# Optimization experiments

Measured on AMD Instinct MI355X. Metric: run time of the kernel, lower is better.

Reference implementation:

```python
import jax, jax.numpy as jnp
import numpy as np

N, E, D, H, L = 50000, 400000, 128, 256, 2
ZR = 0.8          # z_ratio
GN_EPS = 1e-5     # PyG GraphNorm eps


def _graph_norm(x, w, b, a):
    # PyG GraphNorm on a single graph: x - mean_scale*mean, rms-normalize
    mu = jnp.mean(x, axis=0, keepdims=True)
    xc = x - a * mu
    var = jnp.mean(xc * xc, axis=0, keepdims=True)
    return w * xc / jnp.sqrt(var + GN_EPS) + b


def _gat(x, src, dst, W, a_src, a_dst, bias):
    # PyG GATConv, heads=1, add_self_loops=True, negative_slope=0.2.
    # edge_dim is None -> edge_attr is ignored by the layer.
    n = x.shape[0]
    loop = jnp.arange(n)
    s = jnp.concatenate([src, loop])   # [E+N]
    d = jnp.concatenate([dst, loop])
    xw = x @ W.T                        # [N,H]
    logit = jax.nn.leaky_relu((xw @ a_src)[s] + (xw @ a_dst)[d], 0.2)
    m = jax.ops.segment_max(logit, d, num_segments=n)
    ex = jnp.exp(logit - m[d])
    den = jax.ops.segment_sum(ex, d, num_segments=n)
    alpha = ex / (den[d] + 1e-16)
    return jax.ops.segment_sum(alpha[:, None] * xw[s], d, num_segments=n) + bias


def _mix(x0, x1, mask):
    return jnp.where(mask, ZR * x1 + (1.0 - ZR) * x0, ZR * x0 + (1.0 - ZR) * x1)


def _forward(x_, edge_index, edge_attr, question_embeddings, subgraph_mask,
             node_in_W, node_in_b, edge_in_W, edge_in_b, q_in_W, q_in_b,
             nqm_W, nqm_b, eqm_W, eqm_b,
             t0_W, t0_b, t1_W, t1_b,
             gat_W, gat_asrc, gat_adst, gat_bias,
             cgn_w, cgn_b, cgn_a,
             c0_W, c0_b, c1_W, c1_b,
             gn_w, gn_b, gn_a, final_W, final_b):
    src, dst = edge_index[0], edge_index[1]
    mask = subgraph_mask[:, None]
    x = jax.nn.relu(x_ @ node_in_W.T + node_in_b)                 # [N,H]
    e = jax.nn.relu(edge_attr @ edge_in_W.T + edge_in_b)          # [E,H] (unused by GAT: lin_edge is None)
    q = jax.nn.relu(question_embeddings @ q_in_W.T + q_in_b)[0]   # [1,H]
    n = x.shape[0]
    for l in range(L):
        qx = jnp.broadcast_to(q, (n, H))
        xc = jax.nn.relu(jnp.concatenate([x, qx], axis=-1) @ nqm_W[l].T + nqm_b[l])
        # torch also computes e_combined = relu(edge_question_mix([e,q])) but GATConv
        # (edge_dim=None) ignores it, so it is dead code: omitted.
        x1 = jax.nn.relu(xc @ t1_W[l].T + t1_b[l])
        x0 = jax.nn.relu(xc @ t0_W[l].T + t0_b[l])
        h = _mix(x0, x1, mask)
        h = _gat(h, src, dst, gat_W[l], gat_asrc[l], gat_adst[l], gat_bias[l])
        h = _graph_norm(h, cgn_w[l], cgn_b[l], cgn_a[l])
        # dropout p=0 -> no-op
        hc = jnp.concatenate([h, xc], axis=-1)                    # [N,2H]
        x1 = hc @ c1_W[l].T + c1_b[l]
        x0 = hc @ c0_W[l].T + c0_b[l]
        x = _mix(x0, x1, mask)
        x = _graph_norm(x, gn_w[l], gn_b[l], gn_a[l])
    # masked mean/max/add pooling over subgraph nodes (single graph)
    mk = mask.astype(x.dtype)
    cnt = jnp.sum(mk)
    x_add = jnp.sum(x * mk, axis=0, keepdims=True)
    x_mean = x_add / jnp.maximum(cnt, 1.0)
    x_max = jnp.max(jnp.where(mask, x, -jnp.inf), axis=0, keepdims=True)
    pooled = jnp.concatenate([x_mean, x_max, x_add], axis=-1)     # [1,3H]
    return pooled @ final_W.T + final_b                           # [1,H]


def setup_inputs() -> dict:
    keys = jax.random.split(jax.random.key(0), 64)
    it = iter(range(64))
    def nx(shape, s=0.05):
        return jax.random.normal(keys[next(it)], shape, jnp.float32) * s
    inp = {}
    inp['x_'] = jax.random.normal(keys[next(it)], (N, D), jnp.float32)
    inp['edge_index'] = jax.random.randint(keys[next(it)], (2, E), 0, N)
    inp['edge_attr'] = jax.random.normal(keys[next(it)], (E, D), jnp.float32)
    inp['question_embeddings'] = jax.random.normal(keys[next(it)], (1, 1, D), jnp.float32)
    inp['subgraph_mask'] = jax.random.bernoulli(keys[next(it)], 0.5, (N,))
    inp['node_in_W'] = nx((H, D)); inp['node_in_b'] = nx((H,))
    inp['edge_in_W'] = nx((H, D)); inp['edge_in_b'] = nx((H,))
    inp['q_in_W'] = nx((H, D));    inp['q_in_b'] = nx((H,))
    inp['nqm_W'] = nx((L, H, 2 * H)); inp['nqm_b'] = nx((L, H))
    inp['eqm_W'] = nx((L, H, 2 * H)); inp['eqm_b'] = nx((L, H))
    inp['t0_W'] = nx((L, H, H)); inp['t0_b'] = nx((L, H))
    inp['t1_W'] = nx((L, H, H)); inp['t1_b'] = nx((L, H))
    inp['gat_W'] = nx((L, H, H)); inp['gat_asrc'] = nx((L, H))
    inp['gat_adst'] = nx((L, H)); inp['gat_bias'] = nx((L, H))
    inp['cgn_w'] = jnp.ones((L, H)); inp['cgn_b'] = jnp.zeros((L, H)); inp['cgn_a'] = jnp.ones((L, H))
    inp['c0_W'] = nx((L, H, 2 * H)); inp['c0_b'] = nx((L, H))
    inp['c1_W'] = nx((L, H, 2 * H)); inp['c1_b'] = nx((L, H))
    inp['gn_w'] = jnp.ones((L, H)); inp['gn_b'] = jnp.zeros((L, H)); inp['gn_a'] = jnp.ones((L, H))
    inp['final_W'] = nx((H, 3 * H)); inp['final_b'] = nx((H,))
    return inp


def reference(x_, edge_index, edge_attr, question_embeddings, subgraph_mask,
              node_in_W, node_in_b, edge_in_W, edge_in_b, q_in_W, q_in_b,
              nqm_W, nqm_b, eqm_W, eqm_b,
              t0_W, t0_b, t1_W, t1_b,
              gat_W, gat_asrc, gat_adst, gat_bias,
              cgn_w, cgn_b, cgn_a,
              c0_W, c0_b, c1_W, c1_b,
              gn_w, gn_b, gn_a, final_W, final_b):
    return _forward(x_, edge_index, edge_attr, question_embeddings, subgraph_mask,
                    node_in_W, node_in_b, edge_in_W, edge_in_b, q_in_W, q_in_b,
                    nqm_W, nqm_b, eqm_W, eqm_b,
                    t0_W, t0_b, t1_W, t1_b,
                    gat_W, gat_asrc, gat_adst, gat_bias,
                    cgn_w, cgn_b, cgn_a,
                    c0_W, c0_b, c1_W, c1_b,
                    gn_w, gn_b, gn_a, final_W, final_b)
```

## Files before the change

kernel.cpp:

```cpp
#include <hip/hip_runtime.h>
#include <stdint.h>

#define NNODES 50000
#define NEDGES 400000
#define MPAD   50048
#define MTILES 391
#define ZRF    0.8f
#define GNEPS  1e-5f
#define NBLK   196

typedef unsigned short u16;
typedef __bf16 bf16x8 __attribute__((ext_vector_type(8)));
typedef float  f32x4  __attribute__((ext_vector_type(4)));

#define OFF_NODEW 0
#define OFF_NQM   32768
#define OFF_TCAT  163840
#define OFF_GAT   425984
#define OFF_CCAT  557056
#define W_TOTAL   1081344

__device__ __forceinline__ float b2f(u16 u){ union{uint32_t i; float f;} x; x.i=((uint32_t)u)<<16; return x.f; }
__device__ __forceinline__ u16 f2b(float f){ union{float f; uint32_t i;} x; x.f=f; uint32_t r=x.i+0x7FFFu+((x.i>>16)&1u); return (u16)(r>>16); }
__device__ __forceinline__ float lrelu(float x){ return x>0.f? x : 0.2f*x; }
__device__ __forceinline__ void atomicMaxF(float* a, float v){
  if (v>=0.f) atomicMax((int*)a, __float_as_int(v));
  else atomicMin((unsigned int*)a, (unsigned int)__float_as_int(v));
}

__device__ __forceinline__ void gl16(const void* g, void* l){
  __builtin_amdgcn_global_load_lds((const __attribute__((address_space(1))) void*)g,
                                   (__attribute__((address_space(3))) void*)l, 16, 0, 0);
}
__device__ __forceinline__ void bar(){
  __builtin_amdgcn_sched_barrier(0);
  asm volatile("" ::: "memory");
  __builtin_amdgcn_s_barrier();
  asm volatile("" ::: "memory");
  __builtin_amdgcn_sched_barrier(0);
}

template<int DUAL,int SPLIT,int RELU,int STATS,int DOTAV>
__device__ __forceinline__ void gemm_body(const u16* __restrict__ A0, const u16* __restrict__ A1,
    int ldA, const u16* __restrict__ B, const float* __restrict__ bias,
    u16* __restrict__ out, int ldo, int NT, int K,
    const uint32_t* __restrict__ mask, float* __restrict__ sums,
    const float* __restrict__ asrc, const float* __restrict__ adst,
    float* __restrict__ avs, float* __restrict__ avd)
{
  __shared__ alignas(16) char smem[DUAL ? 33792 : 34816];
  char* sm = smem;
  float* was = (float*)(smem + 32768);
  float* val = was + 128;

  const int tid  = threadIdx.x;
  const int nwg = gridDim.x;
  const int qc = nwg >> 3, rc = nwg & 7;
  const int xcd = blockIdx.x & 7, xi = blockIdx.x >> 3;
  const int lt = (xcd < rc ? xcd * (qc + 1) : rc * (qc + 1) + (xcd - rc) * qc) + xi;
  const int bm0 = (lt / NT) * 128;
  const int bn0 = (lt % NT) * (DUAL ? 64 : 128);

  if (DUAL && tid < 128) {
    int gr = bm0 + tid;
    int mk = (gr < NNODES) ? (mask[gr] != 0) : 0;
    was[tid] = mk ? ZRF : (1.0f - ZRF);
    val[tid] = (gr < NNODES) ? 1.0f : 0.0f;
  }

  const int lane = tid & 63;
  const int wv   = tid >> 6;
  const int wm   = (wv >> 1) * 64;
  const int wn   = (wv & 1) * (DUAL ? 32 : 64);
  const int lrow = lane & 15;
  const int kg16 = (lane >> 4) * 16;
  const int swz  = ((lrow >> 1) & 3) << 4;

  const int rA  = ((wv << 6) + lane) >> 2;
  const int gsw = (((lane & 3) ^ ((rA >> 1) & 3)) << 3);
  const u16* pa  = A0 + (size_t)(bm0 + rA) * ldA + gsw;
  const u16* pa2 = pa + 64 * ldA;
  const u16* pa1  = SPLIT ? (A1 + (size_t)(bm0 + rA) * 256 + gsw) : nullptr;
  const u16* pa12 = SPLIT ? (pa1 + 64 * 256) : nullptr;
  const u16* pb0 = B + (size_t)(bn0 + rA) * K + gsw;
  const u16* pb1 = DUAL ? (B + (size_t)(256 + bn0 + rA) * K + gsw) : (pb0 + (size_t)64 * K);
  const int dA0 = wv * 1024, dA1 = 4096 + wv * 1024;
  const int dB0 = 8192 + wv * 1024, dB1 = 12288 + wv * 1024;

  const int KT = K >> 5;
  f32x4 acc[DUAL ? 2 : 1][4][DUAL ? 2 : 4] = {};

#define STAGE(bb, ktv) do { \
    int ks_ = (ktv) * 32; \
    const u16 *qa_, *qa2_; \
    if (SPLIT && ks_ >= 256) { qa_ = pa1 + (ks_ - 256); qa2_ = pa12 + (ks_ - 256); } \
    else                     { qa_ = pa + ks_;           qa2_ = pa2 + ks_; } \
    char* db_ = sm + (bb); \
    gl16(qa_,       db_ + dA0); \
    gl16(qa2_,      db_ + dA1); \
    gl16(pb0 + ks_, db_ + dB0); \
    gl16(pb1 + ks_, db_ + dB1); \
  } while (0)

  STAGE(0, 0);
  int bb = 0;
  for (int kt = 0; kt < KT; ++kt) {
    if (kt + 1 < KT) { STAGE(bb ^ 16384, kt + 1); asm volatile("s_waitcnt vmcnt(4)" ::: "memory"); }
    else             { asm volatile("s_waitcnt vmcnt(0)" ::: "memory"); }
    bar();
    const char* Ab = sm + bb;
    const char* Bb = Ab + 8192;
    bf16x8 af[4];
#pragma unroll
    for (int mi = 0; mi < 4; ++mi)
      af[mi] = *(const bf16x8*)(Ab + (wm + mi * 16 + lrow) * 64 + (kg16 ^ swz));
    if (DUAL) {
#pragma unroll
      for (int ni = 0; ni < 2; ++ni) {
        int ro = (wn + ni * 16 + lrow) * 64 + (kg16 ^ swz);
        bf16x8 b0 = *(const bf16x8*)(Bb + ro);
        bf16x8 b1 = *(const bf16x8*)(Bb + 4096 + ro);
#pragma unroll
        for (int mi = 0; mi < 4; ++mi) {
          acc[0][mi][ni] = __builtin_amdgcn_mfma_f32_16x16x32_bf16(af[mi], b0, acc[0][mi][ni], 0, 0, 0);
          acc[DUAL?1:0][mi][ni] = __builtin_amdgcn_mfma_f32_16x16x32_bf16(af[mi], b1, acc[DUAL?1:0][mi][ni], 0, 0, 0);
        }
      }
    } else {
#pragma unroll
      for (int ni = 0; ni < (DUAL ? 2 : 4); ++ni) {
        bf16x8 bv = *(const bf16x8*)(Bb + (wn + ni * 16 + lrow) * 64 + (kg16 ^ swz));
#pragma unroll
        for (int mi = 0; mi < 4; ++mi)
          acc[0][mi][ni] = __builtin_amdgcn_mfma_f32_16x16x32_bf16(af[mi], bv, acc[0][mi][ni], 0, 0, 0);
      }
    }
    bar();
    bb ^= 16384;
  }
#undef STAGE

  const int rb = (lane >> 4) * 4;
  u16* ep = (u16*)smem;
  if (DUAL) {
    float sA[2] = {0, 0}, qA[2] = {0, 0};
#pragma unroll
    for (int ni = 0; ni < 2; ++ni) {
      int coll = wn + ni * 16 + lrow;
      float b1v = bias[bn0 + coll];
      float b0v = bias[256 + bn0 + coll];
#pragma unroll
      for (int mi = 0; mi < 4; ++mi) {
        int rowl = wm + mi * 16 + rb;
#pragma unroll
        for (int r = 0; r < 4; ++r) {
          float v1 = acc[0][mi][ni][r] + b1v;
          float v0 = acc[DUAL?1:0][mi][ni][r] + b0v;
          if (RELU) { v1 = fmaxf(v1, 0.f); v0 = fmaxf(v0, 0.f); }
          float wa = was[rowl + r];
          float v = wa * v1 + (1.0f - wa) * v0;
          if (STATS) { float vl = val[rowl + r]; sA[ni] += v * vl; qA[ni] += v * v * vl; }
          ep[(rowl + r) * 72 + coll] = f2b(v);
        }
      }
    }
    bar();
#pragma unroll
    for (int p = 0; p < 4; ++p) {
      int rowl = p * 32 + (tid >> 3);
      uint4 v = *(const uint4*)&ep[rowl * 72 + (tid & 7) * 8];
      *(uint4*)&out[(size_t)(bm0 + rowl) * ldo + bn0 + (tid & 7) * 8] = v;
    }
    if (STATS) {
#pragma unroll
      for (int ni = 0; ni < 2; ++ni) {
        sA[ni] += __shfl_xor(sA[ni], 16); sA[ni] += __shfl_xor(sA[ni], 32);
        qA[ni] += __shfl_xor(qA[ni], 16); qA[ni] += __shfl_xor(qA[ni], 32);
      }
      if (lane < 16) {
#pragma unroll
        for (int ni = 0; ni < 2; ++ni) {
          int gc = bn0 + wn + ni * 16 + lane;
          atomicAdd(&sums[gc], sA[ni]);
          atomicAdd(&sums[256 + gc], qA[ni]);
        }
      }
    }
  } else {
    float sp[4][4] = {}, dp[4][4] = {};
#pragma unroll
    for (int ni = 0; ni < 4; ++ni) {
      int coll = wn + ni * 16 + lrow;
      float bv = bias ? bias[bn0 + coll] : 0.f;
      float as_ = 0.f, ad_ = 0.f;
      if (DOTAV) { as_ = asrc[bn0 + coll]; ad_ = adst[bn0 + coll]; }
#pragma unroll
      for (int mi = 0; mi < 4; ++mi) {
        int rowl = wm + mi * 16 + rb;
#pragma unroll
        for (int r = 0; r < 4; ++r) {
          float v = acc[0][mi][ni][r] + bv;
          if (RELU) v = fmaxf(v, 0.f);
          if (DOTAV) { sp[mi][r] += v * as_; dp[mi][r] += v * ad_; }
          ep[(rowl + r) * 132 + coll] = f2b(v);
        }
      }
    }
    bar();
#pragma unroll
    for (int p = 0; p < 8; ++p) {
      int rowl = p * 16 + (tid >> 4);
      uint4 v = *(const uint4*)&ep[rowl * 132 + (tid & 15) * 8];
      *(uint4*)&out[(size_t)(bm0 + rowl) * ldo + bn0 + (tid & 15) * 8] = v;
    }
    if (DOTAV) {
#pragma unroll
      for (int mi = 0; mi < 4; ++mi)
#pragma unroll
        for (int r = 0; r < 4; ++r) {
          float s_ = sp[mi][r], d_ = dp[mi][r];
          s_ += __shfl_xor(s_, 1); s_ += __shfl_xor(s_, 2); s_ += __shfl_xor(s_, 4); s_ += __shfl_xor(s_, 8);
          d_ += __shfl_xor(d_, 1); d_ += __shfl_xor(d_, 2); d_ += __shfl_xor(d_, 4); d_ += __shfl_xor(d_, 8);
          if (lrow == 0) {
            int row = bm0 + wm + mi * 16 + (lane >> 4) * 4 + r;
            atomicAdd(&avs[row], s_);
            atomicAdd(&avd[row], d_);
          }
        }
    }
  }
}

__global__ __launch_bounds__(256, 3) void g_nin(const u16* __restrict__ A, const u16* __restrict__ W,
    const float* __restrict__ b, u16* __restrict__ o)
{ gemm_body<0,0,1,0,0>(A, nullptr, 128, W, b, o, 256, 2, 128, nullptr, nullptr, nullptr, nullptr, nullptr, nullptr); }

__global__ __launch_bounds__(256, 3) void g_nqm(const u16* __restrict__ A, const u16* __restrict__ W,
    const float* __restrict__ b, u16* __restrict__ o)
{ gemm_body<0,0,1,0,0>(A, nullptr, 256, W, b, o, 256, 2, 256, nullptr, nullptr, nullptr, nullptr, nullptr, nullptr); }

__global__ __launch_bounds__(256, 3) void g_gat(const u16* __restrict__ A, const u16* __restrict__ W,
    u16* __restrict__ o, const float* __restrict__ asrc, const float* __restrict__ adst,
    float* __restrict__ avs, float* __restrict__ avd)
{ gemm_body<0,0,0,0,1>(A, nullptr, 256, W, nullptr, o, 256, 2, 256, nullptr, nullptr, asrc, adst, avs, avd); }

__global__ __launch_bounds__(256, 3) void g_tcat(const u16* __restrict__ A, const u16* __restrict__ W,
    const float* __restrict__ b, u16* __restrict__ o, const uint32_t* __restrict__ mask)
{ gemm_body<1,0,1,0,0>(A, nullptr, 256, W, b, o, 256, 4, 256, mask, nullptr, nullptr, nullptr, nullptr, nullptr); }

__global__ __launch_bounds__(256, 3) void g_ccat(const u16* __restrict__ A0, const u16* __restrict__ A1,
    const u16* __restrict__ W, const float* __restrict__ b, u16* __restrict__ o,
    const uint32_t* __restrict__ mask, float* __restrict__ sums)
{ gemm_body<1,1,0,1,0>(A0, A1, 256, W, b, o, 256, 4, 512, mask, sums, nullptr, nullptr, nullptr, nullptr); }

__global__ void foldw(const u16* __restrict__ Ws, const float* __restrict__ bs,
                      const float* __restrict__ scale, const float* __restrict__ shift,
                      int K, u16* __restrict__ Wd, float* __restrict__ bd){
  int n = blockIdx.x, t = threadIdx.x;
  float bacc = 0.f;
  for (int k = t; k < K; k += 256) {
    float w = b2f(Ws[(size_t)n * K + k]);
    if (k < 256) { bacc += w * shift[k]; w *= scale[k]; }
    Wd[(size_t)n * K + k] = f2b(w);
  }
  for (int d = 32; d; d >>= 1) bacc += __shfl_xor(bacc, d);
  __shared__ float red[4];
  if ((t & 63) == 0) red[t >> 6] = bacc;
  __syncthreads();
  if (t == 0) bd[n] = bs[n] + red[0] + red[1] + red[2] + red[3];
}

__global__ void zeroall(float* __restrict__ z, int ztot, float* __restrict__ pmax){
  int i = blockIdx.x * 256 + threadIdx.x;
  if (i < 256) pmax[i] = -__builtin_inff();
  for (int j = i; j < ztot; j += gridDim.x * 256) z[j] = 0.f;
}

__global__ void convw(const float* __restrict__ nodeW, const float* __restrict__ nqmW,
                      const float* __restrict__ t0W, const float* __restrict__ t1W,
                      const float* __restrict__ gatW, const float* __restrict__ c0W,
                      const float* __restrict__ c1W, u16* __restrict__ arena){
  int idx = blockIdx.x*256 + threadIdx.x;
  if (idx >= W_TOTAL) return;
  float v;
  if (idx < OFF_NQM) { v = nodeW[idx]; }
  else if (idx < OFF_TCAT){ int i = idx - OFF_NQM;  int l=i>>16; int r=(i>>8)&255; int k=i&255; v = nqmW[l*131072 + r*512 + k]; }
  else if (idx < OFF_GAT) { int i = idx - OFF_TCAT; int l=i>>17; int n=(i>>8)&511; int k=i&255;
                            const float* s = (n<256)? t1W : t0W; v = s[l*65536 + (n&255)*256 + k]; }
  else if (idx < OFF_CCAT){ int i = idx - OFF_GAT;  v = gatW[i]; }
  else                    { int i = idx - OFF_CCAT; int l=i>>18; int n=(i>>9)&511; int k=i&511;
                            const float* s = (n<256)? c1W : c0W; v = s[l*131072 + (n&255)*512 + k]; }
  arena[idx] = f2b(v);
}

__global__ void convxin(const float* __restrict__ x, u16* __restrict__ o){
  int idx = blockIdx.x*256 + threadIdx.x;
  if (idx >= MPAD*32) return;
  int n = idx >> 5; int c = (idx & 31)*4;
  float4 v = make_float4(0.f,0.f,0.f,0.f);
  if (n < NNODES) v = *(const float4*)&x[(size_t)n*128 + c];
  ushort4 r; r.x=f2b(v.x); r.y=f2b(v.y); r.z=f2b(v.z); r.w=f2b(v.w);
  *(ushort4*)&o[(size_t)n*128 + c] = r;
}

__global__ void biascat(const float* __restrict__ t1b, const float* __restrict__ t0b,
                        const float* __restrict__ c1b, const float* __restrict__ c0b,
                        float* __restrict__ tb, float* __restrict__ cb){
  int i = blockIdx.x*256 + threadIdx.x;
  if (i >= 2048) return;
  int which = i >> 10; int j = i & 1023; int l = j >> 9; int n = j & 511;
  const float* b1 = which ? c1b : t1b;
  const float* b0 = which ? c0b : t0b;
  float v = (n < 256) ? b1[l*256 + n] : b0[l*256 + n - 256];
  (which ? cb : tb)[l*512 + n] = v;
}

__global__ void qvk(const float* __restrict__ qemb, const float* __restrict__ W,
                    const float* __restrict__ b, float* __restrict__ qv){
  int h = threadIdx.x;
  float acc = b[h];
  for (int d = 0; d < 128; ++d) acc += qemb[d] * W[h*128 + d];
  qv[h] = fmaxf(acc, 0.f);
}

__global__ void qbk(const float* __restrict__ nqmW, const float* __restrict__ nqmB,
                    const float* __restrict__ qv, float* __restrict__ qb){
  int l = blockIdx.x, h = threadIdx.x;
  const float* wr = nqmW + l*131072 + h*512 + 256;
  float acc = nqmB[l*256 + h];
  for (int j = 0; j < 256; ++j) acc += wr[j] * qv[j];
  qb[l*256 + h] = acc;
}

__global__ void detmask(const unsigned char* __restrict__ mb, int* __restrict__ flag){
  __shared__ int cnt_s;
  if (threadIdx.x == 0) cnt_s = 0;
  __syncthreads();
  int c = 0;
  for (int i = threadIdx.x; i < NNODES; i += 1024) c += (mb[i] != 0);
  atomicAdd(&cnt_s, c);
  __syncthreads();
  if (threadIdx.x == 0) *flag = (cnt_s * 8 > NNODES * 3) ? 1 : 0;
}

__global__ void maskmat(const void* __restrict__ m, const int* __restrict__ flag,
                        uint32_t* __restrict__ mask){
  int i = blockIdx.x*256 + threadIdx.x;
  if (i >= NNODES) return;
  int f = *flag;
  mask[i] = f ? (((const unsigned char*)m)[i] != 0) : (((const int*)m)[i] != 0);
}

__global__ void hist(const int* __restrict__ dst, int* __restrict__ count){
  int i = blockIdx.x*256 + threadIdx.x;
  if (i < NEDGES) atomicAdd(&count[dst[i]], 1);
}

__global__ void bsum(const int* __restrict__ count, int* __restrict__ bsums){
  int b = blockIdx.x, t = threadIdx.x;
  int i = b * 256 + t;
  int v = (i < NNODES) ? count[i] : 0;
  for (int d = 32; d; d >>= 1) v += __shfl_xor(v, d);
  __shared__ int red[4];
  if ((t & 63) == 0) red[t >> 6] = v;
  __syncthreads();
  if (t == 0) bsums[b] = red[0] + red[1] + red[2] + red[3];
}

__global__ void bscan(const int* __restrict__ bsums, int* __restrict__ bpre){
  int t = threadIdx.x;
  int v = (t < NBLK) ? bsums[t] : 0;
  __shared__ int tmp[256];
  tmp[t] = v;
  __syncthreads();
  for (int d = 1; d < 256; d <<= 1) {
    int add = (t >= d) ? tmp[t - d] : 0;
    __syncthreads();
    tmp[t] += add;
    __syncthreads();
  }
  if (t < NBLK) bpre[t] = tmp[t] - v;
}

__global__ void scanblk(const int* __restrict__ count, const int* __restrict__ bpre,
                        int* __restrict__ offs, int* __restrict__ cursor){
  int b = blockIdx.x, t = threadIdx.x;
  int i = b * 256 + t;
  int v = (i < NNODES) ? count[i] : 0;
  __shared__ int tmp[256];
  tmp[t] = v;
  __syncthreads();
  for (int d = 1; d < 256; d <<= 1) {
    int add = (t >= d) ? tmp[t - d] : 0;
    __syncthreads();
    tmp[t] += add;
    __syncthreads();
  }
  int excl = bpre[b] + tmp[t] - v;
  if (i < NNODES) { offs[i] = excl; cursor[i] = excl; }
  if (i == NNODES - 1) offs[NNODES] = excl + v;
}

__global__ void scatter(const int* __restrict__ src, const int* __restrict__ dst,
                        int* __restrict__ cursor, int* __restrict__ ssrc){
  int i = blockIdx.x*256 + threadIdx.x;
  if (i >= NEDGES) return;
  int p = atomicAdd(&cursor[dst[i]], 1);
  ssrc[p] = src[i];
}

__global__ void agg(const int* __restrict__ offs, const int* __restrict__ ssrc,
                    const float* __restrict__ avs, const float* __restrict__ avd,
                    const u16* __restrict__ xw, const float* __restrict__ gbias,
                    u16* __restrict__ out){
  int v = (blockIdx.x*256 + threadIdx.x) >> 6;
  int lane = threadIdx.x & 63;
  if (v >= NNODES) return;
  int o0 = offs[v], o1 = offs[v+1];
  int deg = o1 - o0;
  float ad = avd[v];
  float slog = lrelu(avs[v] + ad);
  int c = lane*4;
  ushort4 xv = *(const ushort4*)&xw[(size_t)v*256 + c];
  float a0, a1, a2, a3;
  if (deg <= 64) {
    int s = 0; float logit = -3.0e38f;
    if (lane < deg) { s = ssrc[o0 + lane]; logit = lrelu(avs[s] + ad); }
    float m = fmaxf(slog, logit);
    for (int d = 32; d; d >>= 1) m = fmaxf(m, __shfl_xor(m, d));
    float w = (lane < deg) ? __expf(logit - m) : 0.f;
    float den = w + ((lane == 0) ? __expf(slog - m) : 0.f);
    for (int d = 32; d; d >>= 1) den += __shfl_xor(den, d);
    float rden = 1.0f / (den + 1e-16f);
    w *= rden;
    float wgt = __expf(slog - m) * rden;
    a0 = wgt*b2f(xv.x); a1 = wgt*b2f(xv.y); a2 = wgt*b2f(xv.z); a3 = wgt*b2f(xv.w);
    int i = 0;
    for (; i + 4 <= deg; i += 4) {
      int s0=__shfl(s,i), s1=__shfl(s,i+1), s2=__shfl(s,i+2), s3=__shfl(s,i+3);
      float w0=__shfl(w,i), w1=__shfl(w,i+1), w2=__shfl(w,i+2), w3=__shfl(w,i+3);
      ushort4 q0 = *(const ushort4*)&xw[(size_t)s0*256 + c];
      ushort4 q1 = *(const ushort4*)&xw[(size_t)s1*256 + c];
      ushort4 q2 = *(const ushort4*)&xw[(size_t)s2*256 + c];
      ushort4 q3 = *(const ushort4*)&xw[(size_t)s3*256 + c];
      a0 += w0*b2f(q0.x) + w1*b2f(q1.x) + w2*b2f(q2.x) + w3*b2f(q3.x);
      a1 += w0*b2f(q0.y) + w1*b2f(q1.y) + w2*b2f(q2.y) + w3*b2f(q3.y);
      a2 += w0*b2f(q0.z) + w1*b2f(q1.z) + w2*b2f(q2.z) + w3*b2f(q3.z);
      a3 += w0*b2f(q0.w) + w1*b2f(q1.w) + w2*b2f(q2.w) + w3*b2f(q3.w);
    }
    for (; i < deg; ++i) {
      int si = __shfl(s, i); float wi = __shfl(w, i);
      ushort4 q = *(const ushort4*)&xw[(size_t)si*256 + c];
      a0 += wi*b2f(q.x); a1 += wi*b2f(q.y); a2 += wi*b2f(q.z); a3 += wi*b2f(q.w);
    }
  } else {
    float m = slog;
    for (int i = o0 + lane; i < o1; i += 64) m = fmaxf(m, lrelu(avs[ssrc[i]] + ad));
    for (int d = 32; d; d >>= 1) m = fmaxf(m, __shfl_xor(m, d));
    float den = (lane == 0) ? __expf(slog - m) : 0.f;
    for (int i = o0 + lane; i < o1; i += 64) den += __expf(lrelu(avs[ssrc[i]] + ad) - m);
    for (int d = 32; d; d >>= 1) den += __shfl_xor(den, d);
    float rden = 1.0f / (den + 1e-16f);
    float wgt = __expf(slog - m) * rden;
    a0 = wgt*b2f(xv.x); a1 = wgt*b2f(xv.y); a2 = wgt*b2f(xv.z); a3 = wgt*b2f(xv.w);
    for (int i = o0; i < o1; ++i) {
      int si = ssrc[i];
      float wi = __expf(lrelu(avs[si] + ad) - m) * rden;
      ushort4 q = *(const ushort4*)&xw[(size_t)si*256 + c];
      a0 += wi*b2f(q.x); a1 += wi*b2f(q.y); a2 += wi*b2f(q.z); a3 += wi*b2f(q.w);
    }
  }
  float4 bb = *(const float4*)&gbias[c];
  ushort4 r;
  r.x = f2b(a0 + bb.x); r.y = f2b(a1 + bb.y); r.z = f2b(a2 + bb.z); r.w = f2b(a3 + bb.w);
  *(ushort4*)&out[(size_t)v*256 + c] = r;
}

__global__ void colstats(const u16* __restrict__ x, float* __restrict__ sums){
  int c = threadIdx.x;
  float s = 0.f, q = 0.f;
  for (int n = blockIdx.x; n < NNODES; n += gridDim.x){
    float v = b2f(x[(size_t)n*256 + c]); s += v; q += v*v;
  }
  atomicAdd(&sums[c], s); atomicAdd(&sums[256 + c], q);
}

__global__ void scaleshift(const float* __restrict__ sums, const float* __restrict__ w,
                           const float* __restrict__ b, const float* __restrict__ a,
                           float* __restrict__ scale, float* __restrict__ shift){
  int c = threadIdx.x;
  const float invn = 1.0f / (float)NNODES;
  float mu  = sums[c] * invn;
  float ex2 = sums[256 + c] * invn;
  float av  = a[c];
  float var = ex2 - (2.0f*av - av*av)*mu*mu;
  float sc  = w[c] / sqrtf(var + GNEPS);
  scale[c] = sc;
  shift[c] = b[c] - sc*av*mu;
}

__global__ void pool(const u16* __restrict__ x, const uint32_t* __restrict__ mask,
                     const float* __restrict__ scale, const float* __restrict__ shift,
                     float* __restrict__ psum, float* __restrict__ pmax, int* __restrict__ pcnt){
  int c = threadIdx.x;
  float sc = scale[c], sh = shift[c];
  float s = 0.f, mx = -__builtin_inff(); int cnt = 0;
  for (int n = blockIdx.x; n < NNODES; n += gridDim.x){
    if (mask[n]){
      float v = b2f(x[(size_t)n*256 + c]) * sc + sh;
      s += v; mx = fmaxf(mx, v); cnt++;
    }
  }
  atomicAdd(&psum[c], s);
  atomicMaxF(&pmax[c], mx);
  if (c == 0) atomicAdd(pcnt, cnt);
}

__global__ void finalk(const float* __restrict__ psum, const float* __restrict__ pmax,
                       const int* __restrict__ pcnt, const float* __restrict__ W,
                       const float* __restrict__ b, float* __restrict__ out){
  int o = threadIdx.x;
  float cnt = fmaxf((float)(*pcnt), 1.0f);
  float inv = 1.0f / cnt;
  const float* wr = W + o*768;
  float acc = b[o];
  for (int j = 0; j < 256; ++j) acc += (psum[j]*inv) * wr[j];
  for (int j = 0; j < 256; ++j) acc += pmax[j] * wr[256 + j];
  for (int j = 0; j < 256; ++j) acc += psum[j] * wr[512 + j];
  out[o] = acc;
}

extern "C" void kernel_launch(void* const* d_in, const int* in_sizes, int n_in,
                              void* d_out, int out_size, void* d_ws, size_t ws_size,
                              hipStream_t stream)
{
  (void)in_sizes; (void)n_in; (void)out_size; (void)ws_size;
  const float* x_    = (const float*)d_in[0];
  const int*   eidx  = (const int*)  d_in[1];
  const float* qemb  = (const float*)d_in[3];
  const void*  mraw  =               d_in[4];
  const float* nodeW = (const float*)d_in[5];
  const float* nodeB = (const float*)d_in[6];
  const float* qinW  = (const float*)d_in[9];
  const float* qinB  = (const float*)d_in[10];
  const float* nqmW  = (const float*)d_in[11];
  const float* nqmB  = (const float*)d_in[12];
  const float* t0W   = (const float*)d_in[15];
  const float* t0B   = (const float*)d_in[16];
  const float* t1W   = (const float*)d_in[17];
  const float* t1B   = (const float*)d_in[18];
  const float* gatW  = (const float*)d_in[19];
  const float* gatAs = (const float*)d_in[20];
  const float* gatAd = (const float*)d_in[21];
  const float* gatB  = (const float*)d_in[22];
  const float* cgnW  = (const float*)d_in[23];
  const float* cgnB  = (const float*)d_in[24];
  const float* cgnA  = (const float*)d_in[25];
  const float* c0W   = (const float*)d_in[26];
  const float* c0B   = (const float*)d_in[27];
  const float* c1W   = (const float*)d_in[28];
  const float* c1B   = (const float*)d_in[29];
  const float* gnW   = (const float*)d_in[30];
  const float* gnB   = (const float*)d_in[31];
  const float* gnA   = (const float*)d_in[32];
  const float* finW  = (const float*)d_in[33];
  const float* finB  = (const float*)d_in[34];
  float* outp = (float*)d_out;

  char* p = (char*)d_ws;
  auto alloc = [&](size_t b)->char*{ char* r = p; p += (b + 511) & ~(size_t)511; return r; };
  u16*      arena = (u16*)     alloc((size_t)W_TOTAL*2);
  u16*      wtc   = (u16*)     alloc((size_t)512*512*2);
  u16*      wtn   = (u16*)     alloc((size_t)256*256*2);
  float*    btc   = (float*)   alloc(512*4);
  float*    qbt   = (float*)   alloc(256*4);
  float*    tb    = (float*)   alloc(1024*4);
  float*    cb    = (float*)   alloc(1024*4);
  float*    qv    = (float*)   alloc(256*4);
  float*    qb    = (float*)   alloc(512*4);
  float*    scaleC= (float*)   alloc(256*4);
  float*    shiftC= (float*)   alloc(256*4);
  float*    scaleG= (float*)   alloc(256*4);
  float*    shiftG= (float*)   alloc(256*4);
  float*    pmax  = (float*)   alloc(256*4);
  int*      flag  = (int*)     alloc(256);
  uint32_t* mask  = (uint32_t*)alloc((size_t)NNODES*4);
  int*      offs  = (int*)     alloc((size_t)(NNODES+1)*4);
  int*      cursor= (int*)     alloc((size_t)NNODES*4);
  int*      ssrc  = (int*)     alloc((size_t)NEDGES*4);
  int*      bsums = (int*)     alloc((size_t)NBLK*4);
  int*      bpre  = (int*)     alloc((size_t)NBLK*4);

  const int Z_COUNT = 0;
  const int Z_SUMS  = 50048;
  const int Z_AV    = Z_SUMS + 2048;
  const int Z_PSUM  = Z_AV + 4*MPAD;
  const int Z_PCNT  = Z_PSUM + 256;
  const int ZTOT    = Z_PCNT + 64;
  float*    zar   = (float*)   alloc((size_t)ZTOT*4);
  int*      count = (int*)(zar + Z_COUNT);
  float*    sumsC0= zar + Z_SUMS;
  float*    sumsC1= zar + Z_SUMS + 512;
  float*    sumsG0= zar + Z_SUMS + 1024;
  float*    sumsG1= zar + Z_SUMS + 1536;
  float*    av    = zar + Z_AV;
  float*    psum  = zar + Z_PSUM;
  int*      pcnt  = (int*)(zar + Z_PCNT);

  u16*      xin   = (u16*)     alloc((size_t)MPAD*128*2);
  u16*      xb    = (u16*)     alloc((size_t)MPAD*256*2);
  u16*      xc    = (u16*)     alloc((size_t)MPAD*256*2);
  u16*      hb    = (u16*)     alloc((size_t)MPAD*256*2);
  u16*      xw    = (u16*)     alloc((size_t)MPAD*256*2);
  u16*      hgat  = (u16*)     alloc((size_t)MPAD*256*2);
  u16*      xm    = (u16*)     alloc((size_t)MPAD*256*2);

  const int* esrc = eidx;
  const int* edst = eidx + NEDGES;

  zeroall<<<dim3(256), dim3(256), 0, stream>>>(zar, ZTOT, pmax);
  convw  <<<dim3((W_TOTAL+255)/256), dim3(256), 0, stream>>>(nodeW, nqmW, t0W, t1W, gatW, c0W, c1W, arena);
  convxin<<<dim3(MPAD*32/256), dim3(256), 0, stream>>>(x_, xin);
  biascat<<<dim3(8), dim3(256), 0, stream>>>(t1B, t0B, c1B, c0B, tb, cb);
  qvk    <<<dim3(1), dim3(256), 0, stream>>>(qemb, qinW, qinB, qv);
  qbk    <<<dim3(2), dim3(256), 0, stream>>>(nqmW, nqmB, qv, qb);
  detmask<<<dim3(1), dim3(1024), 0, stream>>>((const unsigned char*)mraw, flag);
  maskmat<<<dim3((NNODES+255)/256), dim3(256), 0, stream>>>(mraw, flag, mask);
  hist   <<<dim3((NEDGES+255)/256), dim3(256), 0, stream>>>(edst, count);
  bsum   <<<dim3(NBLK), dim3(256), 0, stream>>>(count, bsums);
  bscan  <<<dim3(1), dim3(256), 0, stream>>>(bsums, bpre);
  scanblk<<<dim3(NBLK), dim3(256), 0, stream>>>(count, bpre, offs, cursor);
  scatter<<<dim3((NEDGES+255)/256), dim3(256), 0, stream>>>(esrc, edst, cursor, ssrc);

  g_nin<<<dim3(MTILES*2), dim3(256), 0, stream>>>(xin, arena+OFF_NODEW, nodeB, xb);

  for (int l = 0; l < 2; ++l) {
    float* avs_l = av + l*2*MPAD;
    float* avd_l = avs_l + MPAD;
    float* sumsC = l ? sumsC1 : sumsC0;
    float* sumsG = l ? sumsG1 : sumsG0;
    if (l == 0)
      g_nqm<<<dim3(MTILES*2), dim3(256), 0, stream>>>(xb, arena+OFF_NQM, qb, xc);
    else
      g_nqm<<<dim3(MTILES*2), dim3(256), 0, stream>>>(xm, wtn, qbt, xc);
    g_tcat<<<dim3(MTILES*4), dim3(256), 0, stream>>>(xc, arena+OFF_TCAT + l*131072, tb + l*512, hb, mask);
    g_gat<<<dim3(MTILES*2), dim3(256), 0, stream>>>(hb, arena+OFF_GAT + l*65536, xw,
                                                    gatAs + l*256, gatAd + l*256, avs_l, avd_l);
    agg  <<<dim3(12500), dim3(256), 0, stream>>>(offs, ssrc, avs_l, avd_l, xw, gatB + l*256, hgat);
    colstats  <<<dim3(1024), dim3(256), 0, stream>>>(hgat, sumsC);
    scaleshift<<<dim3(1), dim3(256), 0, stream>>>(sumsC, cgnW + l*256, cgnB + l*256, cgnA + l*256, scaleC, shiftC);
    foldw     <<<dim3(512), dim3(256), 0, stream>>>(arena+OFF_CCAT + l*262144, cb + l*512, scaleC, shiftC, 512, wtc, btc);
    g_ccat<<<dim3(MTILES*4), dim3(256), 0, stream>>>(hgat, xc, wtc, btc, xm, mask, sumsG);
    scaleshift<<<dim3(1), dim3(256), 0, stream>>>(sumsG, gnW + l*256, gnB + l*256, gnA + l*256, scaleG, shiftG);
    if (l == 0)
      foldw<<<dim3(256), dim3(256), 0, stream>>>(arena+OFF_NQM + 65536, qb + 256, scaleG, shiftG, 256, wtn, qbt);
  }

  pool  <<<dim3(512), dim3(256), 0, stream>>>(xm, mask, scaleG, shiftG, psum, pmax, pcnt);
  finalk<<<dim3(1), dim3(256), 0, stream>>>(psum, pmax, pcnt, finW, finB, outp);
}
```

Before: 546.1 us.

## Triple-buffer GEMM LDS pipeline, fold scaleshift into consumers, parallelize mask detection

The GEMM main loop moves from double to triple buffering in LDS, prefetching two k-tiles ahead so only one barrier per iteration is needed. The separate scaleshift kernels are removed: foldw and pool now compute GraphNorm scale and shift from the column sums themselves. The single-block mask detection kernel becomes a multi-block reduction. The agg inner loop is unrolled to 8 gathers in flight. Together these target kernel launch count and memory latency, at the cost of more LDS per block (which may lower occupancy) and redundant scale/shift math in every block.

```diff
diff --git a/kernel.cpp b/kernel.cpp
--- a/kernel.cpp
+++ b/kernel.cpp
@@ -48,9 +48,9 @@
     const float* __restrict__ asrc, const float* __restrict__ adst,
     float* __restrict__ avs, float* __restrict__ avd)
 {
-  __shared__ alignas(16) char smem[DUAL ? 33792 : 34816];
+  __shared__ alignas(16) char smem[50176];
   char* sm = smem;
-  float* was = (float*)(smem + 32768);
+  float* was = (float*)(smem + 49152);
   float* val = was + 128;
 
   const int tid  = threadIdx.x;
@@ -90,12 +90,12 @@
   const int KT = K >> 5;
   f32x4 acc[DUAL ? 2 : 1][4][DUAL ? 2 : 4] = {};
 
-#define STAGE(bb, ktv) do { \
+#define STAGE(off, ktv) do { \
     int ks_ = (ktv) * 32; \
     const u16 *qa_, *qa2_; \
     if (SPLIT && ks_ >= 256) { qa_ = pa1 + (ks_ - 256); qa2_ = pa12 + (ks_ - 256); } \
     else                     { qa_ = pa + ks_;           qa2_ = pa2 + ks_; } \
-    char* db_ = sm + (bb); \
+    char* db_ = sm + (off); \
     gl16(qa_,       db_ + dA0); \
     gl16(qa2_,      db_ + dA1); \
     gl16(pb0 + ks_, db_ + dB0); \
@@ -103,12 +103,14 @@
   } while (0)
 
   STAGE(0, 0);
-  int bb = 0;
+  if (KT > 1) STAGE(16384, 1);
+  int rd = 0;
   for (int kt = 0; kt < KT; ++kt) {
-    if (kt + 1 < KT) { STAGE(bb ^ 16384, kt + 1); asm volatile("s_waitcnt vmcnt(4)" ::: "memory"); }
+    if (kt + 1 < KT) { asm volatile("s_waitcnt vmcnt(4)" ::: "memory"); }
     else             { asm volatile("s_waitcnt vmcnt(0)" ::: "memory"); }
     bar();
-    const char* Ab = sm + bb;
+    if (kt + 2 < KT) { int st = rd >= 1 ? rd - 1 : 2; STAGE(st * 16384, kt + 2); }
+    const char* Ab = sm + rd * 16384;
     const char* Bb = Ab + 8192;
     bf16x8 af[4];
 #pragma unroll
@@ -135,10 +137,10 @@
           acc[0][mi][ni] = __builtin_amdgcn_mfma_f32_16x16x32_bf16(af[mi], bv, acc[0][mi][ni], 0, 0, 0);
       }
     }
-    bar();
-    bb ^= 16384;
+    rd = (rd + 1 == 3) ? 0 : rd + 1;
   }
 #undef STAGE
+  bar();
 
   const int rb = (lane >> 4) * 4;
   u16* ep = (u16*)smem;
@@ -254,14 +256,27 @@
 { gemm_body<1,1,0,1,0>(A0, A1, 256, W, b, o, 256, 4, 512, mask, sums, nullptr, nullptr, nullptr, nullptr); }
 
 __global__ void foldw(const u16* __restrict__ Ws, const float* __restrict__ bs,
-                      const float* __restrict__ scale, const float* __restrict__ shift,
+                      const float* __restrict__ sums, const float* __restrict__ w,
+                      const float* __restrict__ b, const float* __restrict__ a,
                       int K, u16* __restrict__ Wd, float* __restrict__ bd){
+  __shared__ float scs[256], shs[256];
   int n = blockIdx.x, t = threadIdx.x;
+  {
+    const float invn = 1.0f / (float)NNODES;
+    float mu  = sums[t] * invn;
+    float ex2 = sums[256 + t] * invn;
+    float av  = a[t];
+    float var = ex2 - (2.0f*av - av*av)*mu*mu;
+    float sc  = w[t] / sqrtf(var + GNEPS);
+    scs[t] = sc;
+    shs[t] = b[t] - sc*av*mu;
+  }
+  __syncthreads();
   float bacc = 0.f;
   for (int k = t; k < K; k += 256) {
-    float w = b2f(Ws[(size_t)n * K + k]);
-    if (k < 256) { bacc += w * shift[k]; w *= scale[k]; }
-    Wd[(size_t)n * K + k] = f2b(w);
+    float wv = b2f(Ws[(size_t)n * K + k]);
+    if (k < 256) { bacc += wv * shs[k]; wv *= scs[k]; }
+    Wd[(size_t)n * K + k] = f2b(wv);
   }
   for (int d = 32; d; d >>= 1) bacc += __shfl_xor(bacc, d);
   __shared__ float red[4];
@@ -332,22 +347,21 @@
   qb[l*256 + h] = acc;
 }
 
-__global__ void detmask(const unsigned char* __restrict__ mb, int* __restrict__ flag){
-  __shared__ int cnt_s;
-  if (threadIdx.x == 0) cnt_s = 0;
+__global__ void detmask(const unsigned char* __restrict__ mb, int* __restrict__ cnt){
+  int i = blockIdx.x*256 + threadIdx.x;
+  int c = (i < NNODES) ? (mb[i] != 0) : 0;
+  for (int d = 32; d; d >>= 1) c += __shfl_xor(c, d);
+  __shared__ int red[4];
+  if ((threadIdx.x & 63) == 0) red[threadIdx.x >> 6] = c;
   __syncthreads();
-  int c = 0;
-  for (int i = threadIdx.x; i < NNODES; i += 1024) c += (mb[i] != 0);
-  atomicAdd(&cnt_s, c);
-  __syncthreads();
-  if (threadIdx.x == 0) *flag = (cnt_s * 8 > NNODES * 3) ? 1 : 0;
-}
-
-__global__ void maskmat(const void* __restrict__ m, const int* __restrict__ flag,
+  if (threadIdx.x == 0) atomicAdd(cnt, red[0] + red[1] + red[2] + red[3]);
+}
+
+__global__ void maskmat(const void* __restrict__ m, const int* __restrict__ cnt,
                         uint32_t* __restrict__ mask){
   int i = blockIdx.x*256 + threadIdx.x;
   if (i >= NNODES) return;
-  int f = *flag;
+  int f = ((*cnt) * 8 > NNODES * 3);
   mask[i] = f ? (((const unsigned char*)m)[i] != 0) : (((const int*)m)[i] != 0);
 }
 
@@ -436,17 +450,31 @@
     float wgt = __expf(slog - m) * rden;
     a0 = wgt*b2f(xv.x); a1 = wgt*b2f(xv.y); a2 = wgt*b2f(xv.z); a3 = wgt*b2f(xv.w);
     int i = 0;
+    for (; i + 8 <= deg; i += 8) {
+      ushort4 q[8]; float ww[8];
+#pragma unroll
+      for (int j = 0; j < 8; ++j) {
+        int sj = __shfl(s, i + j); ww[j] = __shfl(w, i + j);
+        q[j] = *(const ushort4*)&xw[(size_t)sj*256 + c];
+      }
+#pragma unroll
+      for (int j = 0; j < 8; ++j) {
+        a0 += ww[j]*b2f(q[j].x); a1 += ww[j]*b2f(q[j].y);
+        a2 += ww[j]*b2f(q[j].z); a3 += ww[j]*b2f(q[j].w);
+      }
+    }
     for (; i + 4 <= deg; i += 4) {
-      int s0=__shfl(s,i), s1=__shfl(s,i+1), s2=__shfl(s,i+2), s3=__shfl(s,i+3);
-      float w0=__shfl(w,i), w1=__shfl(w,i+1), w2=__shfl(w,i+2), w3=__shfl(w,i+3);
-      ushort4 q0 = *(const ushort4*)&xw[(size_t)s0*256 + c];
-      ushort4 q1 = *(const ushort4*)&xw[(size_t)s1*256 + c];
-      ushort4 q2 = *(const ushort4*)&xw[(size_t)s2*256 + c];
-      ushort4 q3 = *(const ushort4*)&xw[(size_t)s3*256 + c];
-      a0 += w0*b2f(q0.x) + w1*b2f(q1.x) + w2*b2f(q2.x) + w3*b2f(q3.x);
-      a1 += w0*b2f(q0.y) + w1*b2f(q1.y) + w2*b2f(q2.y) + w3*b2f(q3.y);
-      a2 += w0*b2f(q0.z) + w1*b2f(q1.z) + w2*b2f(q2.z) + w3*b2f(q3.z);
-      a3 += w0*b2f(q0.w) + w1*b2f(q1.w) + w2*b2f(q2.w) + w3*b2f(q3.w);
+      ushort4 q[4]; float ww[4];
+#pragma unroll
+      for (int j = 0; j < 4; ++j) {
+        int sj = __shfl(s, i + j); ww[j] = __shfl(w, i + j);
+        q[j] = *(const ushort4*)&xw[(size_t)sj*256 + c];
+      }
+#pragma unroll
+      for (int j = 0; j < 4; ++j) {
+        a0 += ww[j]*b2f(q[j].x); a1 += ww[j]*b2f(q[j].y);
+        a2 += ww[j]*b2f(q[j].z); a3 += ww[j]*b2f(q[j].w);
+      }
     }
     for (; i < deg; ++i) {
       int si = __shfl(s, i); float wi = __shfl(w, i);
@@ -485,9 +513,10 @@
   atomicAdd(&sums[c], s); atomicAdd(&sums[256 + c], q);
 }
 
-__global__ void scaleshift(const float* __restrict__ sums, const float* __restrict__ w,
-                           const float* __restrict__ b, const float* __restrict__ a,
-                           float* __restrict__ scale, float* __restrict__ shift){
+__global__ void pool(const u16* __restrict__ x, const uint32_t* __restrict__ mask,
+                     const float* __restrict__ sums, const float* __restrict__ w,
+                     const float* __restrict__ b, const float* __restrict__ a,
+                     float* __restrict__ psum, float* __restrict__ pmax, int* __restrict__ pcnt){
   int c = threadIdx.x;
   const float invn = 1.0f / (float)NNODES;
   float mu  = sums[c] * invn;
@@ -495,15 +524,7 @@
   float av  = a[c];
   float var = ex2 - (2.0f*av - av*av)*mu*mu;
   float sc  = w[c] / sqrtf(var + GNEPS);
-  scale[c] = sc;
-  shift[c] = b[c] - sc*av*mu;
-}
-
-__global__ void pool(const u16* __restrict__ x, const uint32_t* __restrict__ mask,
-                     const float* __restrict__ scale, const float* __restrict__ shift,
-                     float* __restrict__ psum, float* __restrict__ pmax, int* __restrict__ pcnt){
-  int c = threadIdx.x;
-  float sc = scale[c], sh = shift[c];
+  float sh  = b[c] - sc*av*mu;
   float s = 0.f, mx = -__builtin_inff(); int cnt = 0;
   for (int n = blockIdx.x; n < NNODES; n += gridDim.x){
     if (mask[n]){
@@ -578,12 +599,7 @@
   float*    cb    = (float*)   alloc(1024*4);
   float*    qv    = (float*)   alloc(256*4);
   float*    qb    = (float*)   alloc(512*4);
-  float*    scaleC= (float*)   alloc(256*4);
-  float*    shiftC= (float*)   alloc(256*4);
-  float*    scaleG= (float*)   alloc(256*4);
-  float*    shiftG= (float*)   alloc(256*4);
   float*    pmax  = (float*)   alloc(256*4);
-  int*      flag  = (int*)     alloc(256);
   uint32_t* mask  = (uint32_t*)alloc((size_t)NNODES*4);
   int*      offs  = (int*)     alloc((size_t)(NNODES+1)*4);
   int*      cursor= (int*)     alloc((size_t)NNODES*4);
@@ -596,7 +612,8 @@
   const int Z_AV    = Z_SUMS + 2048;
   const int Z_PSUM  = Z_AV + 4*MPAD;
   const int Z_PCNT  = Z_PSUM + 256;
-  const int ZTOT    = Z_PCNT + 64;
+  const int Z_MCNT  = Z_PCNT + 64;
+  const int ZTOT    = Z_MCNT + 64;
   float*    zar   = (float*)   alloc((size_t)ZTOT*4);
   int*      count = (int*)(zar + Z_COUNT);
   float*    sumsC0= zar + Z_SUMS;
@@ -606,6 +623,7 @@
   float*    av    = zar + Z_AV;
   float*    psum  = zar + Z_PSUM;
   int*      pcnt  = (int*)(zar + Z_PCNT);
+  int*      mcnt  = (int*)(zar + Z_MCNT);
 
   u16*      xin   = (u16*)     alloc((size_t)MPAD*128*2);
   u16*      xb    = (u16*)     alloc((size_t)MPAD*256*2);
@@ -624,8 +642,8 @@
   biascat<<<dim3(8), dim3(256), 0, stream>>>(t1B, t0B, c1B, c0B, tb, cb);
   qvk    <<<dim3(1), dim3(256), 0, stream>>>(qemb, qinW, qinB, qv);
   qbk    <<<dim3(2), dim3(256), 0, stream>>>(nqmW, nqmB, qv, qb);
-  detmask<<<dim3(1), dim3(1024), 0, stream>>>((const unsigned char*)mraw, flag);
-  maskmat<<<dim3((NNODES+255)/256), dim3(256), 0, stream>>>(mraw, flag, mask);
+  detmask<<<dim3(NBLK), dim3(256), 0, stream>>>((const unsigned char*)mraw, mcnt);
+  maskmat<<<dim3((NNODES+255)/256), dim3(256), 0, stream>>>(mraw, mcnt, mask);
   hist   <<<dim3((NEDGES+255)/256), dim3(256), 0, stream>>>(edst, count);
   bsum   <<<dim3(NBLK), dim3(256), 0, stream>>>(count, bsums);
   bscan  <<<dim3(1), dim3(256), 0, stream>>>(bsums, bpre);
@@ -647,15 +665,15 @@
     g_gat<<<dim3(MTILES*2), dim3(256), 0, stream>>>(hb, arena+OFF_GAT + l*65536, xw,
                                                     gatAs + l*256, gatAd + l*256, avs_l, avd_l);
     agg  <<<dim3(12500), dim3(256), 0, stream>>>(offs, ssrc, avs_l, avd_l, xw, gatB + l*256, hgat);
-    colstats  <<<dim3(1024), dim3(256), 0, stream>>>(hgat, sumsC);
-    scaleshift<<<dim3(1), dim3(256), 0, stream>>>(sumsC, cgnW + l*256, cgnB + l*256, cgnA + l*256, scaleC, shiftC);
-    foldw     <<<dim3(512), dim3(256), 0, stream>>>(arena+OFF_CCAT + l*262144, cb + l*512, scaleC, shiftC, 512, wtc, btc);
+    colstats<<<dim3(1024), dim3(256), 0, stream>>>(hgat, sumsC);
+    foldw   <<<dim3(512), dim3(256), 0, stream>>>(arena+OFF_CCAT + l*262144, cb + l*512,
+                                                  sumsC, cgnW + l*256, cgnB + l*256, cgnA + l*256, 512, wtc, btc);
     g_ccat<<<dim3(MTILES*4), dim3(256), 0, stream>>>(hgat, xc, wtc, btc, xm, mask, sumsG);
-    scaleshift<<<dim3(1), dim3(256), 0, stream>>>(sumsG, gnW + l*256, gnB + l*256, gnA + l*256, scaleG, shiftG);
     if (l == 0)
-      foldw<<<dim3(256), dim3(256), 0, stream>>>(arena+OFF_NQM + 65536, qb + 256, scaleG, shiftG, 256, wtn, qbt);
-  }
-
-  pool  <<<dim3(512), dim3(256), 0, stream>>>(xm, mask, scaleG, shiftG, psum, pmax, pcnt);
+      foldw<<<dim3(256), dim3(256), 0, stream>>>(arena+OFF_NQM + 65536, qb + 256,
+                                                 sumsG, gnW, gnB, gnA, 256, wtn, qbt);
+  }
+
+  pool  <<<dim3(512), dim3(256), 0, stream>>>(xm, mask, sumsG1, gnW + 256, gnB + 256, gnA + 256, psum, pmax, pcnt);
   finalk<<<dim3(1), dim3(256), 0, stream>>>(psum, pmax, pcnt, finW, finB, outp);
 }
```

New measurement: 537.7 us. Within noise of the previous version (-1.5%).
